# Performance work log

Hardware: AMD Instinct MI355X
Metric: run time of the kernel (lower is better)

Reference implementation:

```python
import jax, jax.numpy as jnp
import numpy as np
import math


def setup_inputs() -> dict:
    key = jax.random.key(0)
    k1, k2 = jax.random.split(key)
    B, CK, H, W = 4, 128, 64, 64
    Mk = jax.random.normal(k1, (B, CK, H, W), dtype=jnp.float32)
    Qk = jax.random.normal(k2, (B, CK, H, W), dtype=jnp.float32)
    return {"Mk": Mk, "Qk": Qk}


def reference(Mk, Qk):
    B, CK, H, W = Mk.shape
    N = H * W
    mk = Mk.reshape(B, CK, N)   # [B, CK, N_mem]
    qk = Qk.reshape(B, CK, N)   # [B, CK, N_query]
    # squared norm of each memory key: [B, N_mem, 1]
    a_sq = jnp.sum(mk * mk, axis=1)[:, :, None]
    # inner products: [B, N_mem, N_query]
    ab = jnp.einsum('bcm,bcq->bmq', mk, qk)
    affinity = (2.0 * ab - a_sq) / math.sqrt(CK)
    # softmax over memory positions (axis=1), matching F.softmax(dim=1)
    affinity = jax.nn.softmax(affinity, axis=1)
    return affinity
```

## Files before the change

### kernel.cpp

```cpp
#include <hip/hip_runtime.h>
#include <cstdint>

#define CKDIM 128
#define MDIM  4096
#define QDIM  4096
#define BATCH 4

typedef __attribute__((ext_vector_type(8)))  _Float16 half8;
typedef __attribute__((ext_vector_type(4)))  float    f32x4;
typedef __attribute__((ext_vector_type(16))) float    f32x16;

#if __has_builtin(__builtin_amdgcn_exp2f)
#define EXP2(x) __builtin_amdgcn_exp2f(x)
#else
#define EXP2(x) exp2f(x)
#endif

#define ALPHA 0.12753139626596757f
#define K2A   0.25506279253193514f

__device__ inline void gl_lds16(const void* g, void* l) {
    __builtin_amdgcn_global_load_lds(
        (const __attribute__((address_space(1))) unsigned*)g,
        (__attribute__((address_space(3))) unsigned*)l, 16, 0, 0);
}

__global__ void convert_kernel(const float* __restrict__ Mk, const float* __restrict__ Qk,
                               _Float16* __restrict__ At, _Float16* __restrict__ Bt,
                               float* __restrict__ cm, float* __restrict__ sums) {
    __shared__ _Float16 T[128 * 130];
    __shared__ float    asqp[16][128];
    const int blk = blockIdx.x;
    const int mat = blk >> 7;
    const int b   = (blk >> 5) & 3;
    const int t   = blk & 31;
    const float* src = (mat ? Qk : Mk) + (size_t)b * CKDIM * MDIM + t * 128;
    const int tid = threadIdx.x;
    const int kg  = tid >> 4;
    const int ng  = tid & 15;

    float sq[8] = {0.f, 0.f, 0.f, 0.f, 0.f, 0.f, 0.f, 0.f};
    #pragma unroll
    for (int it = 0; it < 8; ++it) {
        int k = it * 16 + kg;
        const float* g = src + (size_t)k * MDIM + ng * 8;
        float4 v0 = *(const float4*)g;
        float4 v1 = *(const float4*)(g + 4);
        _Float16* p = &T[k * 130 + ng * 8];
        p[0] = (_Float16)v0.x; p[1] = (_Float16)v0.y; p[2] = (_Float16)v0.z; p[3] = (_Float16)v0.w;
        p[4] = (_Float16)v1.x; p[5] = (_Float16)v1.y; p[6] = (_Float16)v1.z; p[7] = (_Float16)v1.w;
        if (mat == 0) {
            sq[0] += v0.x * v0.x; sq[1] += v0.y * v0.y;
            sq[2] += v0.z * v0.z; sq[3] += v0.w * v0.w;
            sq[4] += v1.x * v1.x; sq[5] += v1.y * v1.y;
            sq[6] += v1.z * v1.z; sq[7] += v1.w * v1.w;
        }
    }
    if (mat == 0) {
        #pragma unroll
        for (int j = 0; j < 8; ++j) asqp[kg][ng * 8 + j] = sq[j];
    } else {
        if (tid < 128) sums[(blk & 127) * 128 + tid] = 0.f;
    }
    __syncthreads();
    #pragma unroll
    for (int it = 0; it < 8; ++it) {
        int idx = it * 256 + tid;
        int cc  = idx >> 7;
        int n   = idx & 127;
        half8 o;
        #pragma unroll
        for (int j = 0; j < 8; ++j) o[j] = T[(cc * 8 + j) * 130 + n];
        if (mat == 0) {
            _Float16* dst = At + (size_t)b * (MDIM * CKDIM)
                          + (size_t)(t * 2 + (n >> 6)) * 8192 + cc * 512 + (n & 63) * 8;
            *(half8*)dst = o;
        } else {
            _Float16* dst = Bt + (size_t)b * (QDIM * CKDIM)
                          + (size_t)t * 16384 + cc * 1024 + n * 8;
            *(half8*)dst = o;
        }
    }
    if (mat == 0 && tid < 128) {
        float s = 0.f;
        #pragma unroll
        for (int g = 0; g < 16; ++g) s += asqp[g][tid];
        cm[b * MDIM + t * 128 + tid] = -ALPHA * s;
    }
}

template <int WRITE>
__global__ __launch_bounds__(256, 4) void gemm_pass(
        const _Float16* __restrict__ At, const _Float16* __restrict__ Bt,
        const float* __restrict__ cmArr, float* __restrict__ sums,
        float* __restrict__ out) {
    __shared__ __align__(16) char ldsA[2][16384];
    const int tid  = threadIdx.x;
    const int lane = tid & 63;
    const int wv   = tid >> 6;
    const int mg   = wv >> 1;
    const int qg   = wv & 1;
    const int l5   = lane >> 5;
    const int l31  = lane & 31;

    const int wg = blockIdx.x;
    const int id = ((wg & 7) << 7) | (wg >> 3);
    const int b  = id >> 8;
    const int qs = (id >> 3) & 31;
    const int ms = id & 7;
    const int q0 = qs << 7;
    const int m0 = ms << 9;

    const char* Ab = (const char*)At + ((size_t)(b * 64 + ms * 8) << 14);
    const char* Bb = (const char*)Bt + ((size_t)(b * 32 + qs) << 15);

    half8 bq0[8], bq1[8];
    #pragma unroll
    for (int s = 0; s < 8; ++s) {
        const char* p = Bb + (size_t)(2 * s + l5) * 2048 + (qg * 64 + l31) * 16;
        bq0[s] = *(const half8*)(p);
        bq1[s] = *(const half8*)(p + 512);
    }

    float rs0, rs1;
    if (WRITE) {
        rs0 = 1.0f / sums[(b << 12) + q0 + qg * 64 + l31];
        rs1 = 1.0f / sums[(b << 12) + q0 + qg * 64 + 32 + l31];
    }

    #pragma unroll
    for (int r = 0; r < 4; ++r) {
        unsigned Dw = r * 4096u + wv * 1024u;
        gl_lds16(Ab + Dw + lane * 16, ldsA[0] + Dw);
    }
    asm volatile("s_waitcnt vmcnt(0)" ::: "memory");
    __syncthreads();

    const int cmbase = (b << 12) + m0 + mg * 32 + l5 * 4;
    float cs0 = 0.f, cs1 = 0.f;

    #pragma unroll 1
    for (int mt = 0; mt < 8; ++mt) {
        const char* lA = ldsA[mt & 1];
        if (mt + 1 < 8) {
            const char* Asrc = Ab + ((size_t)(mt + 1) << 14);
            char* dst = ldsA[(mt + 1) & 1];
            #pragma unroll
            for (int r = 0; r < 4; ++r) {
                unsigned Dw = r * 4096u + wv * 1024u;
                gl_lds16(Asrc + Dw + lane * 16, dst + Dw);
            }
        }
        __builtin_amdgcn_sched_barrier(0);

        f32x16 acc0 = {}, acc1 = {};
        #pragma unroll
        for (int s = 0; s < 8; ++s) {
            half8 a = *(const half8*)(lA + (2 * s + l5) * 1024 + (mg * 32 + l31) * 16);
            __builtin_amdgcn_s_setprio(1);
            acc0 = __builtin_amdgcn_mfma_f32_32x32x16_f16(a, bq0[s], acc0, 0, 0, 0);
            acc1 = __builtin_amdgcn_mfma_f32_32x32x16_f16(a, bq1[s], acc1, 0, 0, 0);
            __builtin_amdgcn_s_setprio(0);
        }

        if (WRITE) {
            #pragma unroll
            for (int j = 0; j < 4; ++j) {
                f32x4 cmj = *(const f32x4*)&cmArr[cmbase + mt * 64 + j * 8];
                #pragma unroll
                for (int rr = 0; rr < 4; ++rr) {
                    int    row  = m0 + mt * 64 + mg * 32 + j * 8 + rr + l5 * 4;
                    size_t base = ((((size_t)b << 12) + row) << 12) + q0 + qg * 64 + l31;
                    out[base]      = EXP2(fmaf(acc0[j * 4 + rr], K2A, cmj[rr])) * rs0;
                    out[base + 32] = EXP2(fmaf(acc1[j * 4 + rr], K2A, cmj[rr])) * rs1;
                }
            }
        } else {
            #pragma unroll
            for (int j = 0; j < 4; ++j) {
                f32x4 cmj = *(const f32x4*)&cmArr[cmbase + mt * 64 + j * 8];
                #pragma unroll
                for (int rr = 0; rr < 4; ++rr) {
                    cs0 += EXP2(fmaf(acc0[j * 4 + rr], K2A, cmj[rr]));
                    cs1 += EXP2(fmaf(acc1[j * 4 + rr], K2A, cmj[rr]));
                }
            }
        }

        if (mt + 1 < 8) {
            if (WRITE) asm volatile("s_waitcnt vmcnt(36)" ::: "memory");
            else       asm volatile("s_waitcnt vmcnt(4)"  ::: "memory");
            __builtin_amdgcn_s_barrier();
            __builtin_amdgcn_sched_barrier(0);
        }
    }

    if (!WRITE) {
        cs0 += __shfl_xor(cs0, 32);
        cs1 += __shfl_xor(cs1, 32);
        if (lane < 32) {
            __hip_atomic_fetch_add(&sums[(b << 12) + q0 + qg * 64 + lane], cs0,
                                   __ATOMIC_RELAXED, __HIP_MEMORY_SCOPE_AGENT);
            __hip_atomic_fetch_add(&sums[(b << 12) + q0 + qg * 64 + 32 + lane], cs1,
                                   __ATOMIC_RELAXED, __HIP_MEMORY_SCOPE_AGENT);
        }
    }
}

extern "C" void kernel_launch(void* const* d_in, const int* in_sizes, int n_in,
                              void* d_out, int out_size, void* d_ws, size_t ws_size,
                              hipStream_t stream) {
    const float* Mk = (const float*)d_in[0];
    const float* Qk = (const float*)d_in[1];
    float* out = (float*)d_out;

    _Float16* At   = (_Float16*)d_ws;
    _Float16* Bt   = At + (size_t)BATCH * MDIM * CKDIM;
    float*    sums = (float*)(Bt + (size_t)BATCH * MDIM * CKDIM);
    float*    cm   = sums + BATCH * QDIM;

    convert_kernel<<<256, 256, 0, stream>>>(Mk, Qk, At, Bt, cm, sums);
    gemm_pass<0><<<1024, 256, 0, stream>>>(At, Bt, cm, sums, out);
    gemm_pass<1><<<1024, 256, 0, stream>>>(At, Bt, cm, sums, out);
}
```

Before: 84.98 us.

## Drop LDS staging; use 8 waves each loading A fragments directly from global

Removes the LDS double-buffered A tile and its barriers, and moves the GEMM passes to 512-thread blocks. Each of the 8 waves now owns a 32x32 output tile and loads its A fragments straight from global memory into registers. The normalization becomes a log-domain subtraction folded into the exp2 argument, and output is written with nontemporal stores. The aim is to cut synchronization and LDS traffic and to shrink the per-wave register footprint. In exchange, redundant global loads of A across the four q-waves now rely on L1/L2 hits.

```diff
diff --git a/kernel.cpp b/kernel.cpp
--- a/kernel.cpp
+++ b/kernel.cpp
@@ -18,12 +18,6 @@
 
 #define ALPHA 0.12753139626596757f
 #define K2A   0.25506279253193514f
-
-__device__ inline void gl_lds16(const void* g, void* l) {
-    __builtin_amdgcn_global_load_lds(
-        (const __attribute__((address_space(1))) unsigned*)g,
-        (__attribute__((address_space(3))) unsigned*)l, 16, 0, 0);
-}
 
 __global__ void convert_kernel(const float* __restrict__ Mk, const float* __restrict__ Qk,
                                _Float16* __restrict__ At, _Float16* __restrict__ Bt,
@@ -90,16 +84,15 @@
 }
 
 template <int WRITE>
-__global__ __launch_bounds__(256, 4) void gemm_pass(
+__global__ __launch_bounds__(512, 2) void gemm_pass(
         const _Float16* __restrict__ At, const _Float16* __restrict__ Bt,
         const float* __restrict__ cmArr, float* __restrict__ sums,
         float* __restrict__ out) {
-    __shared__ __align__(16) char ldsA[2][16384];
     const int tid  = threadIdx.x;
     const int lane = tid & 63;
     const int wv   = tid >> 6;
-    const int mg   = wv >> 1;
-    const int qg   = wv & 1;
+    const int mg   = wv >> 2;
+    const int qg   = wv & 3;
     const int l5   = lane >> 5;
     const int l31  = lane & 31;
 
@@ -114,65 +107,42 @@
     const char* Ab = (const char*)At + ((size_t)(b * 64 + ms * 8) << 14);
     const char* Bb = (const char*)Bt + ((size_t)(b * 32 + qs) << 15);
 
-    half8 bq0[8], bq1[8];
+    half8 bq[8];
     #pragma unroll
-    for (int s = 0; s < 8; ++s) {
-        const char* p = Bb + (size_t)(2 * s + l5) * 2048 + (qg * 64 + l31) * 16;
-        bq0[s] = *(const half8*)(p);
-        bq1[s] = *(const half8*)(p + 512);
-    }
+    for (int s = 0; s < 8; ++s)
+        bq[s] = *(const half8*)(Bb + (size_t)(2 * s + l5) * 2048 + (qg * 32 + l31) * 16);
 
-    float rs0, rs1;
-    if (WRITE) {
-        rs0 = 1.0f / sums[(b << 12) + q0 + qg * 64 + l31];
-        rs1 = 1.0f / sums[(b << 12) + q0 + qg * 64 + 32 + l31];
-    }
-
-    #pragma unroll
-    for (int r = 0; r < 4; ++r) {
-        unsigned Dw = r * 4096u + wv * 1024u;
-        gl_lds16(Ab + Dw + lane * 16, ldsA[0] + Dw);
-    }
-    asm volatile("s_waitcnt vmcnt(0)" ::: "memory");
-    __syncthreads();
+    float lrs;
+    if (WRITE) lrs = -__log2f(sums[(b << 12) + q0 + qg * 32 + l31]);
 
     const int cmbase = (b << 12) + m0 + mg * 32 + l5 * 4;
-    float cs0 = 0.f, cs1 = 0.f;
+    float cs = 0.f;
 
     #pragma unroll 1
     for (int mt = 0; mt < 8; ++mt) {
-        const char* lA = ldsA[mt & 1];
-        if (mt + 1 < 8) {
-            const char* Asrc = Ab + ((size_t)(mt + 1) << 14);
-            char* dst = ldsA[(mt + 1) & 1];
-            #pragma unroll
-            for (int r = 0; r < 4; ++r) {
-                unsigned Dw = r * 4096u + wv * 1024u;
-                gl_lds16(Asrc + Dw + lane * 16, dst + Dw);
-            }
-        }
-        __builtin_amdgcn_sched_barrier(0);
+        const char* at = Ab + ((size_t)mt << 14) + (mg * 32 + l31) * 16;
+        half8 a[8];
+        #pragma unroll
+        for (int s = 0; s < 8; ++s)
+            a[s] = *(const half8*)(at + (2 * s + l5) * 1024);
 
-        f32x16 acc0 = {}, acc1 = {};
+        f32x16 acc = {};
+        __builtin_amdgcn_s_setprio(1);
         #pragma unroll
-        for (int s = 0; s < 8; ++s) {
-            half8 a = *(const half8*)(lA + (2 * s + l5) * 1024 + (mg * 32 + l31) * 16);
-            __builtin_amdgcn_s_setprio(1);
-            acc0 = __builtin_amdgcn_mfma_f32_32x32x16_f16(a, bq0[s], acc0, 0, 0, 0);
-            acc1 = __builtin_amdgcn_mfma_f32_32x32x16_f16(a, bq1[s], acc1, 0, 0, 0);
-            __builtin_amdgcn_s_setprio(0);
-        }
+        for (int s = 0; s < 8; ++s)
+            acc = __builtin_amdgcn_mfma_f32_32x32x16_f16(a[s], bq[s], acc, 0, 0, 0);
+        __builtin_amdgcn_s_setprio(0);
 
         if (WRITE) {
             #pragma unroll
             for (int j = 0; j < 4; ++j) {
                 f32x4 cmj = *(const f32x4*)&cmArr[cmbase + mt * 64 + j * 8];
+                f32x4 c   = cmj + lrs;
                 #pragma unroll
                 for (int rr = 0; rr < 4; ++rr) {
                     int    row  = m0 + mt * 64 + mg * 32 + j * 8 + rr + l5 * 4;
-                    size_t base = ((((size_t)b << 12) + row) << 12) + q0 + qg * 64 + l31;
-                    out[base]      = EXP2(fmaf(acc0[j * 4 + rr], K2A, cmj[rr])) * rs0;
-                    out[base + 32] = EXP2(fmaf(acc1[j * 4 + rr], K2A, cmj[rr])) * rs1;
+                    size_t base = ((((size_t)b << 12) + row) << 12) + q0 + qg * 32 + l31;
+                    __builtin_nontemporal_store(EXP2(fmaf(acc[j * 4 + rr], K2A, c[rr])), &out[base]);
                 }
             }
         } else {
@@ -180,28 +150,16 @@
             for (int j = 0; j < 4; ++j) {
                 f32x4 cmj = *(const f32x4*)&cmArr[cmbase + mt * 64 + j * 8];
                 #pragma unroll
-                for (int rr = 0; rr < 4; ++rr) {
-                    cs0 += EXP2(fmaf(acc0[j * 4 + rr], K2A, cmj[rr]));
-                    cs1 += EXP2(fmaf(acc1[j * 4 + rr], K2A, cmj[rr]));
-                }
+                for (int rr = 0; rr < 4; ++rr)
+                    cs += EXP2(fmaf(acc[j * 4 + rr], K2A, cmj[rr]));
             }
-        }
-
-        if (mt + 1 < 8) {
-            if (WRITE) asm volatile("s_waitcnt vmcnt(36)" ::: "memory");
-            else       asm volatile("s_waitcnt vmcnt(4)"  ::: "memory");
-            __builtin_amdgcn_s_barrier();
-            __builtin_amdgcn_sched_barrier(0);
         }
     }
 
     if (!WRITE) {
-        cs0 += __shfl_xor(cs0, 32);
-        cs1 += __shfl_xor(cs1, 32);
+        cs += __shfl_xor(cs, 32);
         if (lane < 32) {
-            __hip_atomic_fetch_add(&sums[(b << 12) + q0 + qg * 64 + lane], cs0,
-                                   __ATOMIC_RELAXED, __HIP_MEMORY_SCOPE_AGENT);
-            __hip_atomic_fetch_add(&sums[(b << 12) + q0 + qg * 64 + 32 + lane], cs1,
+            __hip_atomic_fetch_add(&sums[(b << 12) + q0 + qg * 32 + lane], cs,
                                    __ATOMIC_RELAXED, __HIP_MEMORY_SCOPE_AGENT);
         }
     }
@@ -220,6 +178,6 @@
     float*    cm   = sums + BATCH * QDIM;
 
     convert_kernel<<<256, 256, 0, stream>>>(Mk, Qk, At, Bt, cm, sums);
-    gemm_pass<0><<<1024, 256, 0, stream>>>(At, Bt, cm, sums, out);
-    gemm_pass<1><<<1024, 256, 0, stream>>>(At, Bt, cm, sums, out);
+    gemm_pass<0><<<1024, 512, 0, stream>>>(At, Bt, cm, sums, out);
+    gemm_pass<1><<<1024, 512, 0, stream>>>(At, Bt, cm, sums, out);
 }
```

Measured after the change: 107.5 us. 26.5% more time.

## Software-pipeline MFMA halves with epilogue, fold reciprocal into exponent, nontemporal stores

Applied to the files above, without the earlier changes.

Splits each m-tile's two 32x32 accumulations so the epilogue (exp2 and store) of one half runs interleaved with the MFMAs of the other half. It also fully unrolls the m-tile loop and preloads all A fragments from LDS up front. The softmax normalisation is folded into the exponent by adding -log2(sum), replacing a multiply by the reciprocal. Output stores become nontemporal, and launch bounds drop to 3 waves to allow more registers. The changes aim to hide the transcendental and store latency behind matrix work, at the cost of higher register pressure and occupancy, and altered vmcnt wait counts.

```diff
diff --git a/kernel.cpp b/kernel.cpp
--- a/kernel.cpp
+++ b/kernel.cpp
@@ -90,7 +90,7 @@
 }
 
 template <int WRITE>
-__global__ __launch_bounds__(256, 4) void gemm_pass(
+__global__ __launch_bounds__(256, 3) void gemm_pass(
         const _Float16* __restrict__ At, const _Float16* __restrict__ Bt,
         const float* __restrict__ cmArr, float* __restrict__ sums,
         float* __restrict__ out) {
@@ -116,17 +116,41 @@
 
     half8 bq0[8], bq1[8];
     #pragma unroll
-    for (int s = 0; s < 8; ++s) {
-        const char* p = Bb + (size_t)(2 * s + l5) * 2048 + (qg * 64 + l31) * 16;
-        bq0[s] = *(const half8*)(p);
-        bq1[s] = *(const half8*)(p + 512);
-    }
-
-    float rs0, rs1;
+    for (int kk = 0; kk < 8; ++kk) {
+        const char* p = Bb + (size_t)(2 * kk + l5) * 2048 + (qg * 64 + l31) * 16;
+        bq0[kk] = *(const half8*)(p);
+        bq1[kk] = *(const half8*)(p + 512);
+    }
+
+    float lrs0 = 0.f, lrs1 = 0.f;
     if (WRITE) {
-        rs0 = 1.0f / sums[(b << 12) + q0 + qg * 64 + l31];
-        rs1 = 1.0f / sums[(b << 12) + q0 + qg * 64 + 32 + l31];
-    }
+        lrs0 = -__log2f(sums[(b << 12) + q0 + qg * 64 + l31]);
+        lrs1 = -__log2f(sums[(b << 12) + q0 + qg * 64 + 32 + l31]);
+    }
+
+    const int cmbase = (b << 12) + m0 + mg * 32 + l5 * 4;
+    float cs0 = 0.f, cs1 = 0.f;
+
+    auto EP = [&](const f32x16& ac, int t, int h) {
+        #pragma unroll
+        for (int j = 0; j < 4; ++j) {
+            f32x4 cmj = *(const f32x4*)&cmArr[cmbase + t * 64 + j * 8];
+            if (WRITE) {
+                f32x4 c = cmj + (h ? lrs1 : lrs0);
+                #pragma unroll
+                for (int rr = 0; rr < 4; ++rr) {
+                    int    row  = m0 + t * 64 + mg * 32 + j * 8 + rr + l5 * 4;
+                    size_t base = ((((size_t)b << 12) + row) << 12) + q0 + qg * 64 + h * 32 + l31;
+                    __builtin_nontemporal_store(EXP2(fmaf(ac[j * 4 + rr], K2A, c[rr])), &out[base]);
+                }
+            } else {
+                float& cs = h ? cs1 : cs0;
+                #pragma unroll
+                for (int rr = 0; rr < 4; ++rr)
+                    cs += EXP2(fmaf(ac[j * 4 + rr], K2A, cmj[rr]));
+            }
+        }
+    };
 
     #pragma unroll
     for (int r = 0; r < 4; ++r) {
@@ -134,14 +158,13 @@
         gl_lds16(Ab + Dw + lane * 16, ldsA[0] + Dw);
     }
     asm volatile("s_waitcnt vmcnt(0)" ::: "memory");
-    __syncthreads();
-
-    const int cmbase = (b << 12) + m0 + mg * 32 + l5 * 4;
-    float cs0 = 0.f, cs1 = 0.f;
-
-    #pragma unroll 1
+    __builtin_amdgcn_s_barrier();
+
+    const f32x16 ZERO = {};
+    f32x16 accB = ZERO;
+
+    #pragma unroll
     for (int mt = 0; mt < 8; ++mt) {
-        const char* lA = ldsA[mt & 1];
         if (mt + 1 < 8) {
             const char* Asrc = Ab + ((size_t)(mt + 1) << 14);
             char* dst = ldsA[(mt + 1) & 1];
@@ -153,47 +176,41 @@
         }
         __builtin_amdgcn_sched_barrier(0);
 
-        f32x16 acc0 = {}, acc1 = {};
-        #pragma unroll
-        for (int s = 0; s < 8; ++s) {
-            half8 a = *(const half8*)(lA + (2 * s + l5) * 1024 + (mg * 32 + l31) * 16);
-            __builtin_amdgcn_s_setprio(1);
-            acc0 = __builtin_amdgcn_mfma_f32_32x32x16_f16(a, bq0[s], acc0, 0, 0, 0);
-            acc1 = __builtin_amdgcn_mfma_f32_32x32x16_f16(a, bq1[s], acc1, 0, 0, 0);
-            __builtin_amdgcn_s_setprio(0);
-        }
-
-        if (WRITE) {
-            #pragma unroll
-            for (int j = 0; j < 4; ++j) {
-                f32x4 cmj = *(const f32x4*)&cmArr[cmbase + mt * 64 + j * 8];
-                #pragma unroll
-                for (int rr = 0; rr < 4; ++rr) {
-                    int    row  = m0 + mt * 64 + mg * 32 + j * 8 + rr + l5 * 4;
-                    size_t base = ((((size_t)b << 12) + row) << 12) + q0 + qg * 64 + l31;
-                    out[base]      = EXP2(fmaf(acc0[j * 4 + rr], K2A, cmj[rr])) * rs0;
-                    out[base + 32] = EXP2(fmaf(acc1[j * 4 + rr], K2A, cmj[rr])) * rs1;
-                }
-            }
-        } else {
-            #pragma unroll
-            for (int j = 0; j < 4; ++j) {
-                f32x4 cmj = *(const f32x4*)&cmArr[cmbase + mt * 64 + j * 8];
-                #pragma unroll
-                for (int rr = 0; rr < 4; ++rr) {
-                    cs0 += EXP2(fmaf(acc0[j * 4 + rr], K2A, cmj[rr]));
-                    cs1 += EXP2(fmaf(acc1[j * 4 + rr], K2A, cmj[rr]));
-                }
-            }
-        }
+        const char* lA = ldsA[mt & 1];
+        half8 a[8];
+        #pragma unroll
+        for (int kk = 0; kk < 8; ++kk)
+            a[kk] = *(const half8*)(lA + (2 * kk + l5) * 1024 + (mg * 32 + l31) * 16);
+
+        f32x16 accA = ZERO;
+        __builtin_amdgcn_s_setprio(1);
+        #pragma unroll
+        for (int kk = 0; kk < 8; ++kk)
+            accA = __builtin_amdgcn_mfma_f32_32x32x16_f16(a[kk], bq0[kk], accA, 0, 0, 0);
+        __builtin_amdgcn_s_setprio(0);
+        __builtin_amdgcn_sched_barrier(0);
+
+        if (mt > 0) EP(accB, mt - 1, 1);
+        __builtin_amdgcn_sched_barrier(0);
+
+        accB = ZERO;
+        __builtin_amdgcn_s_setprio(1);
+        #pragma unroll
+        for (int kk = 0; kk < 8; ++kk)
+            accB = __builtin_amdgcn_mfma_f32_32x32x16_f16(a[kk], bq1[kk], accB, 0, 0, 0);
+        __builtin_amdgcn_s_setprio(0);
+        __builtin_amdgcn_sched_barrier(0);
+
+        EP(accA, mt, 0);
 
         if (mt + 1 < 8) {
-            if (WRITE) asm volatile("s_waitcnt vmcnt(36)" ::: "memory");
-            else       asm volatile("s_waitcnt vmcnt(4)"  ::: "memory");
+            if (WRITE) asm volatile("s_waitcnt vmcnt(40)" ::: "memory");
+            else       asm volatile("s_waitcnt vmcnt(0)"  ::: "memory");
             __builtin_amdgcn_s_barrier();
             __builtin_amdgcn_sched_barrier(0);
         }
     }
+    EP(accB, 7, 1);
 
     if (!WRITE) {
         cs0 += __shfl_xor(cs0, 32);
```

Result: slower. 121.4 us (+42.8%).
